# Kernel tuning notes

Measured on AMD Instinct MI355X. Metric: run time of the kernel, lower is better.

The kernel has to match this reference:

```python
import jax, jax.numpy as jnp
import numpy as np

B, H, S, D = 2, 16, 2048, 64

def setup_inputs() -> dict:
    key = jax.random.key(0)
    kq, kk, kv = jax.random.split(key, 3)
    Q = jax.random.normal(kq, (B, H, S, D), dtype=jnp.float32)
    K = jax.random.normal(kk, (B, H, S, D), dtype=jnp.float32)
    V = jax.random.normal(kv, (B, H, S, D), dtype=jnp.float32)
    return {"Q": Q, "K": K, "V": V}

def reference(Q, K, V):
    scale = 1.0 / jnp.sqrt(jnp.asarray(Q.shape[-1], dtype=Q.dtype))
    # [B,H,S,S] scores, scaled post-matmul to match torch source
    scores = jnp.einsum('bhqd,bhkd->bhqk', Q, K) * scale
    attn = jax.nn.softmax(scores, axis=-1)
    return jnp.einsum('bhqk,bhkd->bhqd', attn, V)
```

## Files before the change

### kernel.cpp

```cpp
#include <hip/hip_runtime.h>

typedef __bf16 bf16;
typedef __bf16 bf16x4 __attribute__((ext_vector_type(4)));
typedef __bf16 bf16x8 __attribute__((ext_vector_type(8)));
typedef float  f32x4  __attribute__((ext_vector_type(4)));

#define S_LEN 2048
#define DHEAD 64
#define BH    32
#define QB    128
#define KB    64
#define NT    (S_LEN / KB)

static __device__ __forceinline__ void async_cp16(const bf16* g, bf16* l) {
  __builtin_amdgcn_global_load_lds(
      (const __attribute__((address_space(1))) void*)g,
      (__attribute__((address_space(3))) void*)l, 16, 0, 0);
}

static __device__ __forceinline__ f32x4 mfma_bf16(bf16x8 a, bf16x8 b, f32x4 c) {
  return __builtin_amdgcn_mfma_f32_16x16x32_bf16(a, b, c, 0, 0, 0);
}

__global__ __launch_bounds__(256)
void kv_prep(const float* __restrict__ K, const float* __restrict__ V,
             bf16* __restrict__ Kb, bf16* __restrict__ Vt) {
  __shared__ bf16 t[64][72];
  const int bh = blockIdx.x >> 5;
  const int kt = blockIdx.x & 31;
  const int tid = threadIdx.x;
  const size_t tbase = ((size_t)bh * S_LEN + kt * 64) * DHEAD;

  const float* ksrc = K + tbase;
  bf16* kdst = Kb + tbase;
#pragma unroll
  for (int it = 0; it < 2; ++it) {
    const int i = tid + it * 256;
    const float4 a = ((const float4*)ksrc)[2 * i];
    const float4 b = ((const float4*)ksrc)[2 * i + 1];
    bf16x8 o;
    o[0] = (bf16)a.x; o[1] = (bf16)a.y; o[2] = (bf16)a.z; o[3] = (bf16)a.w;
    o[4] = (bf16)b.x; o[5] = (bf16)b.y; o[6] = (bf16)b.z; o[7] = (bf16)b.w;
    ((bf16x8*)kdst)[i] = o;
  }

  const float* vsrc = V + tbase;
  bf16* vdst = Vt + (size_t)bh * DHEAD * S_LEN + kt * 64;
#pragma unroll
  for (int it = 0; it < 4; ++it) {
    const int i = tid + it * 256;
    const int r = i >> 4, c4 = (i & 15) << 2;
    const float4 v = *(const float4*)(vsrc + (size_t)r * DHEAD + c4);
    bf16x4 o;
    o[0] = (bf16)v.x; o[1] = (bf16)v.y; o[2] = (bf16)v.z; o[3] = (bf16)v.w;
    *(bf16x4*)&t[r][c4] = o;
  }
  __syncthreads();
#pragma unroll
  for (int it = 0; it < 2; ++it) {
    const int j = tid + it * 256;
    const int d = j >> 3, c8 = (j & 7) << 3;
    bf16x8 o;
#pragma unroll
    for (int e = 0; e < 8; ++e) o[e] = t[c8 + e][d];
    *(bf16x8*)(vdst + (size_t)d * S_LEN + c8) = o;
  }
}

__global__ __launch_bounds__(512, 4)
void attn_fwd4(const float* __restrict__ Qg0, const bf16* __restrict__ Kb0,
               const bf16* __restrict__ Vt0, float* __restrict__ Og0) {
  __shared__ __align__(16) bf16 Kl[2][KB * DHEAD];
  __shared__ __align__(16) bf16 Vl[2][DHEAD * KB];
  __shared__ __align__(16) bf16 Pl[8][16][64];

  const int tid = threadIdx.x, wid = tid >> 6, lane = tid & 63;
  const int l15 = lane & 15, lg = lane >> 4;
  const int bh = blockIdx.x >> 4;
  const int qb = blockIdx.x & 15;
  const int qbase = qb * QB + wid * 16;

  const float* Qg = Qg0 + (size_t)bh * S_LEN * DHEAD;
  const bf16* Kb = Kb0 + (size_t)bh * S_LEN * DHEAD;
  const bf16* Vt = Vt0 + (size_t)bh * DHEAD * S_LEN;
  float* Og = Og0 + (size_t)bh * S_LEN * DHEAD;

  const int srow = wid * 8 + (lane >> 3);
  const int scl = ((lane & 7) ^ (srow & 7)) << 3;
  const bf16* kg0 = Kb + (size_t)srow * DHEAD + scl;
  const bf16* vg0 = Vt + (size_t)srow * S_LEN + scl;

#define STAGE(b, t)                                  \
  do {                                               \
    async_cp16(kg0 + (size_t)(t) * KB * DHEAD, &Kl[b][wid * 512]); \
    async_cp16(vg0 + (t) * KB, &Vl[b][wid * 512]);   \
  } while (0)

  const float qscale = 0.125f * 1.44269504088896341f;
  bf16x8 qfrag[2];
  {
    const float* qrow = Qg + (size_t)(qbase + l15) * DHEAD;
#pragma unroll
    for (int h = 0; h < 2; ++h) {
      const float* p = qrow + h * 32 + lg * 8;
      const float4 a = *(const float4*)(p);
      const float4 b = *(const float4*)(p + 4);
      bf16x8 f;
      f[0] = (bf16)(a.x * qscale); f[1] = (bf16)(a.y * qscale);
      f[2] = (bf16)(a.z * qscale); f[3] = (bf16)(a.w * qscale);
      f[4] = (bf16)(b.x * qscale); f[5] = (bf16)(b.y * qscale);
      f[6] = (bf16)(b.z * qscale); f[7] = (bf16)(b.w * qscale);
      qfrag[h] = f;
    }
  }

  float m_l = -__builtin_inff();
  float l_l = 0.f;
  f32x4 o_acc[4];
#pragma unroll
  for (int nd = 0; nd < 4; ++nd) o_acc[nd] = f32x4{0.f, 0.f, 0.f, 0.f};

  const int kxor = (l15 & 7) << 4;
  const int pswz = (l15 & 7) << 4;
  char* pbase = (char*)&Pl[wid][0][0] + l15 * 128;

  STAGE(0, 0);
  __syncthreads();

  for (int kt = 0; kt < NT; ++kt) {
    const int cur = kt & 1;
    if (kt + 1 < NT) STAGE(cur ^ 1, kt + 1);

    f32x4 sacc[4] = {};
    __builtin_amdgcn_s_setprio(1);
#pragma unroll
    for (int ns = 0; ns < 4; ++ns) {
      const int krow = ns * 16 + l15;
#pragma unroll
      for (int h = 0; h < 2; ++h) {
        const int kb = krow * 128 + ((((h << 2) + lg) << 4) ^ kxor);
        const bf16x8 kf = *(const bf16x8*)((const char*)&Kl[cur][0] + kb);
        sacc[ns] = mfma_bf16(kf, qfrag[h], sacc[ns]);
      }
    }
    __builtin_amdgcn_s_setprio(0);

    float pmax = sacc[0][0];
#pragma unroll
    for (int ns = 0; ns < 4; ++ns)
#pragma unroll
      for (int r = 0; r < 4; ++r) pmax = fmaxf(pmax, sacc[ns][r]);
    pmax = fmaxf(pmax, __shfl_xor(pmax, 16));
    pmax = fmaxf(pmax, __shfl_xor(pmax, 32));

    if (!__all(pmax <= m_l + 8.f)) {
      const float mn = fmaxf(m_l, pmax);
      const float alpha = __builtin_amdgcn_exp2f(m_l - mn);
      m_l = mn;
      l_l *= alpha;
#pragma unroll
      for (int r = 0; r < 4; ++r) {
        const float a_r = __shfl(alpha, (lane & 48) | (((lane >> 4) & 3) * 4 + r));
        o_acc[0][r] *= a_r;
        o_acc[1][r] *= a_r;
        o_acc[2][r] *= a_r;
        o_acc[3][r] *= a_r;
      }
    }

    float rsum = 0.f;
#pragma unroll
    for (int ns = 0; ns < 4; ++ns) {
#pragma unroll
      for (int r = 0; r < 4; ++r) {
        const float p = __builtin_amdgcn_exp2f(sacc[ns][r] - m_l);
        sacc[ns][r] = p;
        rsum += p;
      }
      bf16x4 pw;
      pw[0] = (bf16)sacc[ns][0]; pw[1] = (bf16)sacc[ns][1];
      pw[2] = (bf16)sacc[ns][2]; pw[3] = (bf16)sacc[ns][3];
      *(bf16x4*)(pbase + (((ns << 5) + (lg << 3)) ^ pswz)) = pw;
    }
    rsum += __shfl_xor(rsum, 16);
    rsum += __shfl_xor(rsum, 32);
    l_l += rsum;

    asm volatile("s_waitcnt lgkmcnt(0)" ::: "memory");

    __builtin_amdgcn_s_setprio(1);
#pragma unroll
    for (int h = 0; h < 2; ++h) {
      const bf16x8 pf = *(const bf16x8*)(pbase + (((h << 6) + (lg << 4)) ^ pswz));
#pragma unroll
      for (int nd = 0; nd < 4; ++nd) {
        const int vrow = nd * 16 + l15;
        const int vb = vrow * 128 + ((((h << 2) + lg) << 4) ^ kxor);
        const bf16x8 vf = *(const bf16x8*)((const char*)&Vl[cur][0] + vb);
        o_acc[nd] = mfma_bf16(pf, vf, o_acc[nd]);
      }
    }
    __builtin_amdgcn_s_setprio(0);
    __syncthreads();
  }

#pragma unroll
  for (int r = 0; r < 4; ++r) {
    const float l_r = __shfl(l_l, (lane & 48) | (((lane >> 4) & 3) * 4 + r));
    const float inv = 1.0f / l_r;
    float* orow = Og + (size_t)(qbase + lg * 4 + r) * DHEAD;
#pragma unroll
    for (int nd = 0; nd < 4; ++nd)
      orow[nd * 16 + l15] = o_acc[nd][r] * inv;
  }
#undef STAGE
}

__global__ __launch_bounds__(256, 2)
void attn_fb(const float* __restrict__ Qg0, const float* __restrict__ Kg0,
             const float* __restrict__ Vg0, float* __restrict__ Og0) {
  __shared__ __align__(16) bf16 Kl[KB][72];
  __shared__ __align__(16) bf16 Vt[DHEAD][72];
  __shared__ __align__(16) bf16 Pl[4][16][72];
  const int tid = threadIdx.x, wid = tid >> 6, lane = tid & 63;
  const int l15 = lane & 15, lg = lane >> 4;
  const int bh = blockIdx.x >> 5, qb = blockIdx.x & 31;
  const int qbase = qb * 64 + wid * 16;
  const size_t base = (size_t)bh * S_LEN * DHEAD;
  const float* Qg = Qg0 + base;
  const float* Kg = Kg0 + base;
  const float* Vg = Vg0 + base;
  float* Og = Og0 + base;
  const float qscale = 0.125f * 1.44269504088896341f;
  bf16x8 qfrag[2];
  {
    const float* qrow = Qg + (size_t)(qbase + l15) * DHEAD;
#pragma unroll
    for (int h = 0; h < 2; ++h) {
      const float* p = qrow + h * 32 + lg * 8;
      const float4 a = *(const float4*)(p);
      const float4 b = *(const float4*)(p + 4);
      bf16x8 f;
      f[0] = (bf16)(a.x * qscale); f[1] = (bf16)(a.y * qscale);
      f[2] = (bf16)(a.z * qscale); f[3] = (bf16)(a.w * qscale);
      f[4] = (bf16)(b.x * qscale); f[5] = (bf16)(b.y * qscale);
      f[6] = (bf16)(b.z * qscale); f[7] = (bf16)(b.w * qscale);
      qfrag[h] = f;
    }
  }
  float m_r[4], l_r[4];
  f32x4 o_acc[4];
#pragma unroll
  for (int r = 0; r < 4; ++r) {
    m_r[r] = -__builtin_inff();
    l_r[r] = 0.f;
    o_acc[r] = f32x4{0.f, 0.f, 0.f, 0.f};
  }
  for (int kt = 0; kt < NT; ++kt) {
    __syncthreads();
#pragma unroll
    for (int it = 0; it < 4; ++it) {
      const int i = tid + it * 256;
      const int row = i >> 4, c4 = (i & 15) << 2;
      const float4 kk = *(const float4*)(Kg + (size_t)(kt * KB + row) * DHEAD + c4);
      bf16x4 kb;
      kb[0] = (bf16)kk.x; kb[1] = (bf16)kk.y; kb[2] = (bf16)kk.z; kb[3] = (bf16)kk.w;
      *(bf16x4*)&Kl[row][c4] = kb;
      const float4 vv = *(const float4*)(Vg + (size_t)(kt * KB + row) * DHEAD + c4);
      Vt[c4 + 0][row] = (bf16)vv.x;
      Vt[c4 + 1][row] = (bf16)vv.y;
      Vt[c4 + 2][row] = (bf16)vv.z;
      Vt[c4 + 3][row] = (bf16)vv.w;
    }
    __syncthreads();
    f32x4 sacc[4] = {};
#pragma unroll
    for (int ns = 0; ns < 4; ++ns)
#pragma unroll
      for (int h = 0; h < 2; ++h) {
        const bf16x8 kf = *(const bf16x8*)&Kl[ns * 16 + l15][h * 32 + lg * 8];
        sacc[ns] = mfma_bf16(qfrag[h], kf, sacc[ns]);
      }
    float rmax[4], alpha[4], rsum[4];
#pragma unroll
    for (int r = 0; r < 4; ++r)
      rmax[r] = fmaxf(fmaxf(sacc[0][r], sacc[1][r]), fmaxf(sacc[2][r], sacc[3][r]));
#pragma unroll
    for (int off = 1; off < 16; off <<= 1)
#pragma unroll
      for (int r = 0; r < 4; ++r)
        rmax[r] = fmaxf(rmax[r], __shfl_xor(rmax[r], off));
#pragma unroll
    for (int r = 0; r < 4; ++r) {
      const float mn = fmaxf(m_r[r], rmax[r]);
      alpha[r] = exp2f(m_r[r] - mn);
      m_r[r] = mn;
      rsum[r] = 0.f;
    }
#pragma unroll
    for (int ns = 0; ns < 4; ++ns)
#pragma unroll
      for (int r = 0; r < 4; ++r) {
        const float p = exp2f(sacc[ns][r] - m_r[r]);
        sacc[ns][r] = p;
        rsum[r] += p;
      }
#pragma unroll
    for (int off = 1; off < 16; off <<= 1)
#pragma unroll
      for (int r = 0; r < 4; ++r)
        rsum[r] += __shfl_xor(rsum[r], off);
#pragma unroll
    for (int r = 0; r < 4; ++r) {
      l_r[r] = l_r[r] * alpha[r] + rsum[r];
      o_acc[0][r] *= alpha[r];
      o_acc[1][r] *= alpha[r];
      o_acc[2][r] *= alpha[r];
      o_acc[3][r] *= alpha[r];
    }
#pragma unroll
    for (int ns = 0; ns < 4; ++ns)
#pragma unroll
      for (int r = 0; r < 4; ++r)
        Pl[wid][lg * 4 + r][ns * 16 + l15] = (bf16)sacc[ns][r];
    asm volatile("s_waitcnt lgkmcnt(0)" ::: "memory");
#pragma unroll
    for (int h = 0; h < 2; ++h) {
      const bf16x8 pf = *(const bf16x8*)&Pl[wid][l15][h * 32 + lg * 8];
#pragma unroll
      for (int nd = 0; nd < 4; ++nd) {
        const bf16x8 vf = *(const bf16x8*)&Vt[nd * 16 + l15][h * 32 + lg * 8];
        o_acc[nd] = mfma_bf16(pf, vf, o_acc[nd]);
      }
    }
  }
#pragma unroll
  for (int r = 0; r < 4; ++r) {
    const float inv = 1.0f / l_r[r];
    float* orow = Og + (size_t)(qbase + lg * 4 + r) * DHEAD;
#pragma unroll
    for (int nd = 0; nd < 4; ++nd)
      orow[nd * 16 + l15] = o_acc[nd][r] * inv;
  }
}

extern "C" void kernel_launch(void* const* d_in, const int* in_sizes, int n_in,
                              void* d_out, int out_size, void* d_ws, size_t ws_size,
                              hipStream_t stream) {
  const float* Q = (const float*)d_in[0];
  const float* K = (const float*)d_in[1];
  const float* V = (const float*)d_in[2];
  float* O = (float*)d_out;

  const size_t elems = (size_t)BH * S_LEN * DHEAD;
  const size_t bf16_bytes = elems * 2;
  if (ws_size >= 2 * bf16_bytes) {
    bf16* Kb = (bf16*)d_ws;
    bf16* Vt = (bf16*)((char*)d_ws + bf16_bytes);
    hipLaunchKernelGGL(kv_prep, dim3(BH * 32), dim3(256), 0, stream, K, V, Kb, Vt);
    hipLaunchKernelGGL(attn_fwd4, dim3(BH * (S_LEN / QB)), dim3(512), 0, stream,
                       Q, Kb, Vt, O);
  } else {
    hipLaunchKernelGGL(attn_fb, dim3(1024), dim3(256), 0, stream, Q, K, V, O);
  }
}
```

Baseline: 142.9 us.

## Process two 16-row query subtiles per wave to reuse K/V LDS fragments

New measurement: 141.9 us. Within noise of the previous version (-0.7%).

```diff
diff --git a/kernel.cpp b/kernel.cpp
--- a/kernel.cpp
+++ b/kernel.cpp
@@ -67,18 +67,18 @@
   }
 }
 
-__global__ __launch_bounds__(512, 4)
-void attn_fwd4(const float* __restrict__ Qg0, const bf16* __restrict__ Kb0,
+__global__ __launch_bounds__(256, 2)
+void attn_fwd5(const float* __restrict__ Qg0, const bf16* __restrict__ Kb0,
                const bf16* __restrict__ Vt0, float* __restrict__ Og0) {
   __shared__ __align__(16) bf16 Kl[2][KB * DHEAD];
   __shared__ __align__(16) bf16 Vl[2][DHEAD * KB];
-  __shared__ __align__(16) bf16 Pl[8][16][64];
+  __shared__ __align__(16) bf16 Pl[4][32][64];
 
   const int tid = threadIdx.x, wid = tid >> 6, lane = tid & 63;
   const int l15 = lane & 15, lg = lane >> 4;
   const int bh = blockIdx.x >> 4;
   const int qb = blockIdx.x & 15;
-  const int qbase = qb * QB + wid * 16;
+  const int qbase = qb * QB + wid * 32;
 
   const float* Qg = Qg0 + (size_t)bh * S_LEN * DHEAD;
   const bf16* Kb = Kb0 + (size_t)bh * S_LEN * DHEAD;
@@ -90,16 +90,21 @@
   const bf16* kg0 = Kb + (size_t)srow * DHEAD + scl;
   const bf16* vg0 = Vt + (size_t)srow * S_LEN + scl;
 
-#define STAGE(b, t)                                  \
-  do {                                               \
-    async_cp16(kg0 + (size_t)(t) * KB * DHEAD, &Kl[b][wid * 512]); \
-    async_cp16(vg0 + (t) * KB, &Vl[b][wid * 512]);   \
+#define STAGE(b, t)                                                  \
+  do {                                                               \
+    const bf16* kg_ = kg0 + (size_t)(t) * KB * DHEAD;                \
+    const bf16* vg_ = vg0 + (t) * KB;                                \
+    async_cp16(kg_, &Kl[b][wid * 512]);                              \
+    async_cp16(kg_ + 32 * DHEAD, &Kl[b][2048 + wid * 512]);          \
+    async_cp16(vg_, &Vl[b][wid * 512]);                              \
+    async_cp16(vg_ + (size_t)32 * S_LEN, &Vl[b][2048 + wid * 512]);  \
   } while (0)
 
   const float qscale = 0.125f * 1.44269504088896341f;
-  bf16x8 qfrag[2];
-  {
-    const float* qrow = Qg + (size_t)(qbase + l15) * DHEAD;
+  bf16x8 qfrag[2][2];
+#pragma unroll
+  for (int rs = 0; rs < 2; ++rs) {
+    const float* qrow = Qg + (size_t)(qbase + rs * 16 + l15) * DHEAD;
 #pragma unroll
     for (int h = 0; h < 2; ++h) {
       const float* p = qrow + h * 32 + lg * 8;
@@ -110,19 +115,22 @@
       f[2] = (bf16)(a.z * qscale); f[3] = (bf16)(a.w * qscale);
       f[4] = (bf16)(b.x * qscale); f[5] = (bf16)(b.y * qscale);
       f[6] = (bf16)(b.z * qscale); f[7] = (bf16)(b.w * qscale);
-      qfrag[h] = f;
-    }
-  }
-
-  float m_l = -__builtin_inff();
-  float l_l = 0.f;
-  f32x4 o_acc[4];
-#pragma unroll
-  for (int nd = 0; nd < 4; ++nd) o_acc[nd] = f32x4{0.f, 0.f, 0.f, 0.f};
+      qfrag[rs][h] = f;
+    }
+  }
+
+  float m_l[2] = {-__builtin_inff(), -__builtin_inff()};
+  float l_l[2] = {0.f, 0.f};
+  f32x4 o_acc[2][4];
+#pragma unroll
+  for (int rs = 0; rs < 2; ++rs)
+#pragma unroll
+    for (int nd = 0; nd < 4; ++nd) o_acc[rs][nd] = f32x4{0.f, 0.f, 0.f, 0.f};
 
   const int kxor = (l15 & 7) << 4;
   const int pswz = (l15 & 7) << 4;
-  char* pbase = (char*)&Pl[wid][0][0] + l15 * 128;
+  char* pbase0 = (char*)&Pl[wid][0][0] + l15 * 128;
+  char* pbase1 = pbase0 + 16 * 128;
 
   STAGE(0, 0);
   __syncthreads();
@@ -131,7 +139,7 @@
     const int cur = kt & 1;
     if (kt + 1 < NT) STAGE(cur ^ 1, kt + 1);
 
-    f32x4 sacc[4] = {};
+    f32x4 sacc[2][4] = {};
     __builtin_amdgcn_s_setprio(1);
 #pragma unroll
     for (int ns = 0; ns < 4; ++ns) {
@@ -140,64 +148,70 @@
       for (int h = 0; h < 2; ++h) {
         const int kb = krow * 128 + ((((h << 2) + lg) << 4) ^ kxor);
         const bf16x8 kf = *(const bf16x8*)((const char*)&Kl[cur][0] + kb);
-        sacc[ns] = mfma_bf16(kf, qfrag[h], sacc[ns]);
+        sacc[0][ns] = mfma_bf16(kf, qfrag[0][h], sacc[0][ns]);
+        sacc[1][ns] = mfma_bf16(kf, qfrag[1][h], sacc[1][ns]);
       }
     }
     __builtin_amdgcn_s_setprio(0);
 
-    float pmax = sacc[0][0];
-#pragma unroll
-    for (int ns = 0; ns < 4; ++ns)
-#pragma unroll
-      for (int r = 0; r < 4; ++r) pmax = fmaxf(pmax, sacc[ns][r]);
-    pmax = fmaxf(pmax, __shfl_xor(pmax, 16));
-    pmax = fmaxf(pmax, __shfl_xor(pmax, 32));
-
-    if (!__all(pmax <= m_l + 8.f)) {
-      const float mn = fmaxf(m_l, pmax);
-      const float alpha = __builtin_amdgcn_exp2f(m_l - mn);
-      m_l = mn;
-      l_l *= alpha;
-#pragma unroll
-      for (int r = 0; r < 4; ++r) {
-        const float a_r = __shfl(alpha, (lane & 48) | (((lane >> 4) & 3) * 4 + r));
-        o_acc[0][r] *= a_r;
-        o_acc[1][r] *= a_r;
-        o_acc[2][r] *= a_r;
-        o_acc[3][r] *= a_r;
-      }
-    }
-
-    float rsum = 0.f;
-#pragma unroll
-    for (int ns = 0; ns < 4; ++ns) {
-#pragma unroll
-      for (int r = 0; r < 4; ++r) {
-        const float p = __builtin_amdgcn_exp2f(sacc[ns][r] - m_l);
-        sacc[ns][r] = p;
-        rsum += p;
-      }
-      bf16x4 pw;
-      pw[0] = (bf16)sacc[ns][0]; pw[1] = (bf16)sacc[ns][1];
-      pw[2] = (bf16)sacc[ns][2]; pw[3] = (bf16)sacc[ns][3];
-      *(bf16x4*)(pbase + (((ns << 5) + (lg << 3)) ^ pswz)) = pw;
-    }
-    rsum += __shfl_xor(rsum, 16);
-    rsum += __shfl_xor(rsum, 32);
-    l_l += rsum;
+#pragma unroll
+    for (int rs = 0; rs < 2; ++rs) {
+      float pmax = sacc[rs][0][0];
+#pragma unroll
+      for (int ns = 0; ns < 4; ++ns)
+#pragma unroll
+        for (int r = 0; r < 4; ++r) pmax = fmaxf(pmax, sacc[rs][ns][r]);
+
+      if (!__all(pmax <= m_l[rs] + 8.f)) {
+        pmax = fmaxf(pmax, __shfl_xor(pmax, 16));
+        pmax = fmaxf(pmax, __shfl_xor(pmax, 32));
+        const float mn = fmaxf(m_l[rs], pmax);
+        const float alpha = __builtin_amdgcn_exp2f(m_l[rs] - mn);
+        m_l[rs] = mn;
+        l_l[rs] *= alpha;
+#pragma unroll
+        for (int r = 0; r < 4; ++r) {
+          const float a_r = __shfl(alpha, (lane & 48) | (((lane >> 4) & 3) * 4 + r));
+          o_acc[rs][0][r] *= a_r;
+          o_acc[rs][1][r] *= a_r;
+          o_acc[rs][2][r] *= a_r;
+          o_acc[rs][3][r] *= a_r;
+        }
+      }
+
+      char* pb = rs ? pbase1 : pbase0;
+      float rsum = 0.f;
+#pragma unroll
+      for (int ns = 0; ns < 4; ++ns) {
+#pragma unroll
+        for (int r = 0; r < 4; ++r) {
+          const float p = __builtin_amdgcn_exp2f(sacc[rs][ns][r] - m_l[rs]);
+          sacc[rs][ns][r] = p;
+          rsum += p;
+        }
+        bf16x4 pw;
+        pw[0] = (bf16)sacc[rs][ns][0]; pw[1] = (bf16)sacc[rs][ns][1];
+        pw[2] = (bf16)sacc[rs][ns][2]; pw[3] = (bf16)sacc[rs][ns][3];
+        *(bf16x4*)(pb + (((ns << 5) + (lg << 3)) ^ pswz)) = pw;
+      }
+      l_l[rs] += rsum;
+    }
 
     asm volatile("s_waitcnt lgkmcnt(0)" ::: "memory");
 
     __builtin_amdgcn_s_setprio(1);
 #pragma unroll
     for (int h = 0; h < 2; ++h) {
-      const bf16x8 pf = *(const bf16x8*)(pbase + (((h << 6) + (lg << 4)) ^ pswz));
+      const int poff = ((h << 6) + (lg << 4)) ^ pswz;
+      const bf16x8 pf0 = *(const bf16x8*)(pbase0 + poff);
+      const bf16x8 pf1 = *(const bf16x8*)(pbase1 + poff);
 #pragma unroll
       for (int nd = 0; nd < 4; ++nd) {
         const int vrow = nd * 16 + l15;
         const int vb = vrow * 128 + ((((h << 2) + lg) << 4) ^ kxor);
         const bf16x8 vf = *(const bf16x8*)((const char*)&Vl[cur][0] + vb);
-        o_acc[nd] = mfma_bf16(pf, vf, o_acc[nd]);
+        o_acc[0][nd] = mfma_bf16(pf0, vf, o_acc[0][nd]);
+        o_acc[1][nd] = mfma_bf16(pf1, vf, o_acc[1][nd]);
       }
     }
     __builtin_amdgcn_s_setprio(0);
@@ -205,13 +219,18 @@
   }
 
 #pragma unroll
-  for (int r = 0; r < 4; ++r) {
-    const float l_r = __shfl(l_l, (lane & 48) | (((lane >> 4) & 3) * 4 + r));
-    const float inv = 1.0f / l_r;
-    float* orow = Og + (size_t)(qbase + lg * 4 + r) * DHEAD;
-#pragma unroll
-    for (int nd = 0; nd < 4; ++nd)
-      orow[nd * 16 + l15] = o_acc[nd][r] * inv;
+  for (int rs = 0; rs < 2; ++rs) {
+    l_l[rs] += __shfl_xor(l_l[rs], 16);
+    l_l[rs] += __shfl_xor(l_l[rs], 32);
+#pragma unroll
+    for (int r = 0; r < 4; ++r) {
+      const float l_r = __shfl(l_l[rs], (lane & 48) | (((lane >> 4) & 3) * 4 + r));
+      const float inv = 1.0f / l_r;
+      float* orow = Og + (size_t)(qbase + rs * 16 + lg * 4 + r) * DHEAD;
+#pragma unroll
+      for (int nd = 0; nd < 4; ++nd)
+        orow[nd * 16 + l15] = o_acc[rs][nd][r] * inv;
+    }
   }
 #undef STAGE
 }
@@ -358,7 +377,7 @@
     bf16* Kb = (bf16*)d_ws;
     bf16* Vt = (bf16*)((char*)d_ws + bf16_bytes);
     hipLaunchKernelGGL(kv_prep, dim3(BH * 32), dim3(256), 0, stream, K, V, Kb, Vt);
-    hipLaunchKernelGGL(attn_fwd4, dim3(BH * (S_LEN / QB)), dim3(512), 0, stream,
+    hipLaunchKernelGGL(attn_fwd5, dim3(BH * (S_LEN / QB)), dim3(256), 0, stream,
                        Q, Kb, Vt, O);
   } else {
     hipLaunchKernelGGL(attn_fb, dim3(1024), dim3(256), 0, stream, Q, K, V, O);
```

## Prepack V into MFMA fragment order and keep P in registers

Applied to the files above, without the earlier changes.

Measured after the change: 141.8 us. No clear change (-0.7%).

```diff
diff --git a/kernel.cpp b/kernel.cpp
--- a/kernel.cpp
+++ b/kernel.cpp
@@ -8,7 +8,7 @@
 #define S_LEN 2048
 #define DHEAD 64
 #define BH    32
-#define QB    128
+#define QB    64
 #define KB    64
 #define NT    (S_LEN / KB)
 
@@ -23,8 +23,8 @@
 }
 
 __global__ __launch_bounds__(256)
-void kv_prep(const float* __restrict__ K, const float* __restrict__ V,
-             bf16* __restrict__ Kb, bf16* __restrict__ Vt) {
+void kv_prep2(const float* __restrict__ K, const float* __restrict__ V,
+              bf16* __restrict__ Kb, bf16* __restrict__ Vf) {
   __shared__ bf16 t[64][72];
   const int bh = blockIdx.x >> 5;
   const int kt = blockIdx.x & 31;
@@ -45,7 +45,6 @@
   }
 
   const float* vsrc = V + tbase;
-  bf16* vdst = Vt + (size_t)bh * DHEAD * S_LEN + kt * 64;
 #pragma unroll
   for (int it = 0; it < 4; ++it) {
     const int i = tid + it * 256;
@@ -56,44 +55,47 @@
     *(bf16x4*)&t[r][c4] = o;
   }
   __syncthreads();
-#pragma unroll
-  for (int it = 0; it < 2; ++it) {
-    const int j = tid + it * 256;
-    const int d = j >> 3, c8 = (j & 7) << 3;
+
+  bf16* vdst = Vf + (size_t)bh * S_LEN * DHEAD + (size_t)kt * 4096;
+  const int lane = tid & 63, nd = tid >> 6;
+  const int lg = lane >> 4, l15 = lane & 15;
+#pragma unroll
+  for (int h = 0; h < 2; ++h) {
     bf16x8 o;
 #pragma unroll
-    for (int e = 0; e < 8; ++e) o[e] = t[c8 + e][d];
-    *(bf16x8*)(vdst + (size_t)d * S_LEN + c8) = o;
-  }
-}
-
-__global__ __launch_bounds__(512, 4)
-void attn_fwd4(const float* __restrict__ Qg0, const bf16* __restrict__ Kb0,
-               const bf16* __restrict__ Vt0, float* __restrict__ Og0) {
+    for (int j = 0; j < 8; ++j)
+      o[j] = t[32 * h + 16 * (j >> 2) + 4 * lg + (j & 3)][nd * 16 + l15];
+    *(bf16x8*)(vdst + ((nd * 2 + h) * 64 + lane) * 8) = o;
+  }
+}
+
+__global__ __launch_bounds__(256, 4)
+void attn_fwd7(const float* __restrict__ Qg0, const bf16* __restrict__ Kb0,
+               const bf16* __restrict__ Vf0, float* __restrict__ Og0) {
   __shared__ __align__(16) bf16 Kl[2][KB * DHEAD];
-  __shared__ __align__(16) bf16 Vl[2][DHEAD * KB];
-  __shared__ __align__(16) bf16 Pl[8][16][64];
 
   const int tid = threadIdx.x, wid = tid >> 6, lane = tid & 63;
   const int l15 = lane & 15, lg = lane >> 4;
-  const int bh = blockIdx.x >> 4;
-  const int qb = blockIdx.x & 15;
+  const int bid = blockIdx.x;
+  const int swz = ((bid & 7) << 7) | (bid >> 3);
+  const int bh = swz >> 5;
+  const int qb = swz & 31;
   const int qbase = qb * QB + wid * 16;
 
   const float* Qg = Qg0 + (size_t)bh * S_LEN * DHEAD;
   const bf16* Kb = Kb0 + (size_t)bh * S_LEN * DHEAD;
-  const bf16* Vt = Vt0 + (size_t)bh * DHEAD * S_LEN;
+  const bf16* Vf = Vf0 + (size_t)bh * S_LEN * DHEAD;
   float* Og = Og0 + (size_t)bh * S_LEN * DHEAD;
 
   const int srow = wid * 8 + (lane >> 3);
   const int scl = ((lane & 7) ^ (srow & 7)) << 3;
   const bf16* kg0 = Kb + (size_t)srow * DHEAD + scl;
-  const bf16* vg0 = Vt + (size_t)srow * S_LEN + scl;
-
-#define STAGE(b, t)                                  \
-  do {                                               \
-    async_cp16(kg0 + (size_t)(t) * KB * DHEAD, &Kl[b][wid * 512]); \
-    async_cp16(vg0 + (t) * KB, &Vl[b][wid * 512]);   \
+
+#define STAGE(b, t)                                            \
+  do {                                                         \
+    const bf16* kg_ = kg0 + (size_t)(t) * KB * DHEAD;          \
+    async_cp16(kg_, &Kl[b][wid * 512]);                        \
+    async_cp16(kg_ + 32 * DHEAD, &Kl[b][2048 + wid * 512]);    \
   } while (0)
 
   const float qscale = 0.125f * 1.44269504088896341f;
@@ -121,8 +123,7 @@
   for (int nd = 0; nd < 4; ++nd) o_acc[nd] = f32x4{0.f, 0.f, 0.f, 0.f};
 
   const int kxor = (l15 & 7) << 4;
-  const int pswz = (l15 & 7) << 4;
-  char* pbase = (char*)&Pl[wid][0][0] + l15 * 128;
+  const bf16* vlane = Vf + lane * 8;
 
   STAGE(0, 0);
   __syncthreads();
@@ -130,6 +131,16 @@
   for (int kt = 0; kt < NT; ++kt) {
     const int cur = kt & 1;
     if (kt + 1 < NT) STAGE(cur ^ 1, kt + 1);
+
+    bf16x8 vf[2][4];
+    {
+      const bf16* vb = vlane + (size_t)kt * 4096;
+#pragma unroll
+      for (int nd = 0; nd < 4; ++nd)
+#pragma unroll
+        for (int h = 0; h < 2; ++h)
+          vf[h][nd] = *(const bf16x8*)(vb + (nd * 2 + h) * 512);
+    }
 
     f32x4 sacc[4] = {};
     __builtin_amdgcn_s_setprio(1);
@@ -150,10 +161,10 @@
     for (int ns = 0; ns < 4; ++ns)
 #pragma unroll
       for (int r = 0; r < 4; ++r) pmax = fmaxf(pmax, sacc[ns][r]);
-    pmax = fmaxf(pmax, __shfl_xor(pmax, 16));
-    pmax = fmaxf(pmax, __shfl_xor(pmax, 32));
 
     if (!__all(pmax <= m_l + 8.f)) {
+      pmax = fmaxf(pmax, __shfl_xor(pmax, 16));
+      pmax = fmaxf(pmax, __shfl_xor(pmax, 32));
       const float mn = fmaxf(m_l, pmax);
       const float alpha = __builtin_amdgcn_exp2f(m_l - mn);
       m_l = mn;
@@ -170,40 +181,36 @@
 
     float rsum = 0.f;
 #pragma unroll
-    for (int ns = 0; ns < 4; ++ns) {
+    for (int ns = 0; ns < 4; ++ns)
 #pragma unroll
       for (int r = 0; r < 4; ++r) {
         const float p = __builtin_amdgcn_exp2f(sacc[ns][r] - m_l);
         sacc[ns][r] = p;
         rsum += p;
       }
-      bf16x4 pw;
-      pw[0] = (bf16)sacc[ns][0]; pw[1] = (bf16)sacc[ns][1];
-      pw[2] = (bf16)sacc[ns][2]; pw[3] = (bf16)sacc[ns][3];
-      *(bf16x4*)(pbase + (((ns << 5) + (lg << 3)) ^ pswz)) = pw;
-    }
-    rsum += __shfl_xor(rsum, 16);
-    rsum += __shfl_xor(rsum, 32);
     l_l += rsum;
 
-    asm volatile("s_waitcnt lgkmcnt(0)" ::: "memory");
+    bf16x8 pa[2];
+#pragma unroll
+    for (int r = 0; r < 4; ++r) {
+      pa[0][r]     = (bf16)sacc[0][r];
+      pa[0][r + 4] = (bf16)sacc[1][r];
+      pa[1][r]     = (bf16)sacc[2][r];
+      pa[1][r + 4] = (bf16)sacc[3][r];
+    }
 
     __builtin_amdgcn_s_setprio(1);
 #pragma unroll
-    for (int h = 0; h < 2; ++h) {
-      const bf16x8 pf = *(const bf16x8*)(pbase + (((h << 6) + (lg << 4)) ^ pswz));
-#pragma unroll
-      for (int nd = 0; nd < 4; ++nd) {
-        const int vrow = nd * 16 + l15;
-        const int vb = vrow * 128 + ((((h << 2) + lg) << 4) ^ kxor);
-        const bf16x8 vf = *(const bf16x8*)((const char*)&Vl[cur][0] + vb);
-        o_acc[nd] = mfma_bf16(pf, vf, o_acc[nd]);
-      }
-    }
+    for (int h = 0; h < 2; ++h)
+#pragma unroll
+      for (int nd = 0; nd < 4; ++nd)
+        o_acc[nd] = mfma_bf16(pa[h], vf[h][nd], o_acc[nd]);
     __builtin_amdgcn_s_setprio(0);
     __syncthreads();
   }
 
+  l_l += __shfl_xor(l_l, 16);
+  l_l += __shfl_xor(l_l, 32);
 #pragma unroll
   for (int r = 0; r < 4; ++r) {
     const float l_r = __shfl(l_l, (lane & 48) | (((lane >> 4) & 3) * 4 + r));
@@ -356,10 +363,10 @@
   const size_t bf16_bytes = elems * 2;
   if (ws_size >= 2 * bf16_bytes) {
     bf16* Kb = (bf16*)d_ws;
-    bf16* Vt = (bf16*)((char*)d_ws + bf16_bytes);
-    hipLaunchKernelGGL(kv_prep, dim3(BH * 32), dim3(256), 0, stream, K, V, Kb, Vt);
-    hipLaunchKernelGGL(attn_fwd4, dim3(BH * (S_LEN / QB)), dim3(512), 0, stream,
-                       Q, Kb, Vt, O);
+    bf16* Vf = (bf16*)((char*)d_ws + bf16_bytes);
+    hipLaunchKernelGGL(kv_prep2, dim3(BH * 32), dim3(256), 0, stream, K, V, Kb, Vf);
+    hipLaunchKernelGGL(attn_fwd7, dim3(BH * (S_LEN / QB)), dim3(256), 0, stream,
+                       Q, Kb, Vf, O);
   } else {
     hipLaunchKernelGGL(attn_fb, dim3(1024), dim3(256), 0, stream, Q, K, V, O);
   }
```
